# Kernel optimization log

Measured on AMD Instinct MI355X. Metric: run time of the kernel, lower is better.

## Reference

```python
import jax, jax.numpy as jnp
import numpy as np

HEAD_NUM = 16
SCALE = 1.0 / np.sqrt(HEAD_NUM)  # source divides by sqrt(head_num), not head_dim
MASK_VAL = -10000000.0


def setup_inputs() -> dict:
    key = jax.random.key(0)
    kq, kk, kv = jax.random.split(key, 3)
    shape = (2, 16, 2048, 64)  # [B, H, L, D]
    Q = jax.random.normal(kq, shape, dtype=jnp.float32)
    K = jax.random.normal(kk, shape, dtype=jnp.float32)
    V = jax.random.normal(kv, shape, dtype=jnp.float32)
    return {"Q": Q, "K": K, "V": V}


def reference(Q, K, V):
    L = Q.shape[-2]
    # [B, H, L, M] attention logits, scaled by 1/sqrt(head_num)
    logits = jnp.einsum('bhld,bhmd->bhlm', Q, K) * SCALE
    # causal mask: strictly-upper triangle gets -1e7 (additive, as in source)
    mask = jnp.triu(jnp.ones((L, L), dtype=logits.dtype), 1) * MASK_VAL
    logits = logits + mask[None, None, :, :]
    weights = jax.nn.softmax(logits, axis=-1)
    return jnp.einsum('bhlm,bhmd->bhld', weights, V)
```

## Files before the change

kernel.cpp:

```cpp
#include <hip/hip_runtime.h>
#include <hip/hip_bf16.h>

#define BM 128
#define BN 64
#define HD 64
#define LQ 2048
#define SD 72

typedef __attribute__((ext_vector_type(8))) short short8;
typedef __attribute__((ext_vector_type(16))) float f32x16;

#define QSCALE 0.360673760222241f

#define WS_HALF  ((size_t)32 * 2048 * 64)
#define WS_NEEDED (2 * WS_HALF * sizeof(unsigned short))

static __device__ __forceinline__ unsigned pk2(float a, float b) {
    union { __hip_bfloat162 h2; unsigned u; } c;
    c.h2 = __float22bfloat162_rn(make_float2(a, b));
    return c.u;
}

__global__ __launch_bounds__(256)
void prep(const float* __restrict__ Kg, const float* __restrict__ Vg,
          unsigned short* __restrict__ KF, unsigned short* __restrict__ VF) {
    __shared__ unsigned short sK2[64][72];
    __shared__ unsigned short sV2[64][72];
    const int t  = threadIdx.x;
    const int bx = blockIdx.x;
    const int bh = bx >> 5;
    const int c  = bx & 31;
    const size_t ibase = (size_t)bh * (LQ * HD) + (size_t)c * 64 * HD;
    const int r  = t >> 4;
    const int c4 = (t & 15) * 4;

#pragma unroll
    for (int p = 0; p < 4; ++p) {
        const int row = p * 16 + r;
        const float4 kv4 = *(const float4*)(Kg + ibase + (size_t)row * HD + c4);
        uint2 ku; ku.x = pk2(kv4.x, kv4.y); ku.y = pk2(kv4.z, kv4.w);
        *(uint2*)&sK2[row][c4] = ku;
        const float4 vv4 = *(const float4*)(Vg + ibase + (size_t)row * HD + c4);
        const unsigned u0 = pk2(vv4.x, vv4.y);
        const unsigned u1 = pk2(vv4.z, vv4.w);
        sV2[c4 + 0][row] = (unsigned short)(u0 & 0xffff);
        sV2[c4 + 1][row] = (unsigned short)(u0 >> 16);
        sV2[c4 + 2][row] = (unsigned short)(u1 & 0xffff);
        sV2[c4 + 3][row] = (unsigned short)(u1 >> 16);
    }
    __syncthreads();

    const int lane = t & 63;
    const int u    = t >> 6;
    const int l31  = lane & 31;
    const int hh   = lane >> 5;
#pragma unroll
    for (int e = 0; e < 2; ++e) {
        const int ch = 2 * c + e;
        const size_t ob = ((size_t)(bh * 64 + ch) * 4 + u) * 512 + lane * 8;
        *(uint4*)&KF[ob] = *(const uint4*)&sK2[e * 32 + l31][u * 16 + hh * 8];
        *(uint4*)&VF[ob] = *(const uint4*)&sV2[(u & 1) * 32 + l31][e * 32 + (u >> 1) * 16 + hh * 8];
    }
}

__global__ __launch_bounds__(512, 4)
void fa_main(const float* __restrict__ Qg,
             const unsigned short* __restrict__ KF,
             const unsigned short* __restrict__ VF,
             float* __restrict__ Og) {
    __shared__ float fx[4 * 64 * 32];
    __shared__ float fla[4 * 32];

    const int t    = threadIdx.x;
    const int w    = t >> 6;
    const int lane = t & 63;
    const int h    = lane >> 5;
    const int l31  = lane & 31;
    const int qg   = w & 3;
    const int kp   = w >> 2;

    const int bx  = blockIdx.x;
    const int bh  = (bx & 7) * 4 + ((bx >> 3) & 3);
    const int g   = bx >> 5;
    const int qt  = (g < 8) ? (15 - g) : (g - 8);

    const size_t base = (size_t)bh * (LQ * HD);
    const unsigned short* KFh = KF + (size_t)bh * 131072 + lane * 8;
    const unsigned short* VFh = VF + (size_t)bh * 131072 + lane * 8;

    const int j    = 4 * qt + qg;
    const int qrow = j * 32 + l31;

    short8 qreg[4];
    {
        const float* Qrow = Qg + base + (size_t)qrow * HD;
#pragma unroll
        for (int ks = 0; ks < 4; ++ks) {
            const float4 a = *(const float4*)(Qrow + ks * 16 + h * 8);
            const float4 b = *(const float4*)(Qrow + ks * 16 + h * 8 + 4);
            union { unsigned u[4]; short8 s8; } qu;
            qu.u[0] = pk2(a.x * QSCALE, a.y * QSCALE);
            qu.u[1] = pk2(a.z * QSCALE, a.w * QSCALE);
            qu.u[2] = pk2(b.x * QSCALE, b.y * QSCALE);
            qu.u[3] = pk2(b.z * QSCALE, b.w * QSCALE);
            qreg[ks] = qu.s8;
        }
    }

    f32x16 accO[2];
#pragma unroll
    for (int r = 0; r < 16; ++r) { accO[0][r] = 0.f; accO[1][r] = 0.f; }
    float lsum = 0.f;

    short8 ak[4], av[4], pf[2];
    f32x16 accS;

    auto loadK = [&](int ch) {
        const unsigned short* p = KFh + (size_t)ch * 2048;
        ak[0] = *(const short8*)(p);
        ak[1] = *(const short8*)(p + 512);
        ak[2] = *(const short8*)(p + 1024);
        ak[3] = *(const short8*)(p + 1536);
    };
    auto loadV = [&](int ch) {
        const unsigned short* p = VFh + (size_t)ch * 2048;
        av[0] = *(const short8*)(p);
        av[1] = *(const short8*)(p + 512);
        av[2] = *(const short8*)(p + 1024);
        av[3] = *(const short8*)(p + 1536);
    };
    auto qkt = [&]() {
#pragma unroll
        for (int r = 0; r < 16; ++r) accS[r] = 0.f;
        __builtin_amdgcn_s_setprio(1);
#pragma unroll
        for (int ks = 0; ks < 4; ++ks)
            accS = __builtin_amdgcn_mfma_f32_32x32x16_bf16(ak[ks], qreg[ks], accS, 0, 0, 0);
        __builtin_amdgcn_s_setprio(0);
    };
    auto smpk = [&](int pc) {
        if (pc == j) {
            const int kvb = pc * 32 + 4 * h;
#pragma unroll
            for (int r = 0; r < 16; ++r) {
                const int kv = kvb + (r & 3) + 8 * (r >> 2);
                if (kv > qrow) accS[r] = -1e30f;
            }
        }
#pragma unroll
        for (int r = 0; r < 16; ++r) {
            const float p = __builtin_amdgcn_exp2f(accS[r]);
            accS[r] = p;
            lsum += p;
        }
#pragma unroll
        for (int s = 0; s < 2; ++s) {
            const int rb = s * 8;
            const unsigned a0 = pk2(accS[rb + 0], accS[rb + 1]);
            const unsigned b0 = pk2(accS[rb + 4], accS[rb + 5]);
            const unsigned a1 = pk2(accS[rb + 2], accS[rb + 3]);
            const unsigned b1 = pk2(accS[rb + 6], accS[rb + 7]);
            const auto r02 = __builtin_amdgcn_permlane32_swap(a0, b0, 0, 0);
            const auto r13 = __builtin_amdgcn_permlane32_swap(a1, b1, 0, 0);
            union { unsigned u[4]; short8 s8; } pu;
            pu.u[0] = r02[0]; pu.u[1] = r13[0]; pu.u[2] = r02[1]; pu.u[3] = r13[1];
            pf[s] = pu.s8;
        }
    };
    auto pv = [&]() {
        __builtin_amdgcn_s_setprio(1);
#pragma unroll
        for (int s = 0; s < 2; ++s)
#pragma unroll
            for (int dg = 0; dg < 2; ++dg)
                accO[dg] = __builtin_amdgcn_mfma_f32_32x32x16_bf16(av[s * 2 + dg], pf[s], accO[dg], 0, 0, 0);
        __builtin_amdgcn_s_setprio(0);
    };

    int ch = kp;
    if (ch <= j) {
        loadK(ch);
        loadV(ch);
        qkt();
        int pc = ch;
        ch += 2;
        while (ch <= j) {
            loadK(ch);
            __builtin_amdgcn_sched_barrier(0);
            smpk(pc);
            pv();
            loadV(ch);
            __builtin_amdgcn_sched_barrier(0);
            qkt();
            pc = ch;
            ch += 2;
        }
        smpk(pc);
        pv();
    }

    lsum += __shfl_xor(lsum, 32);
    if (kp == 1) {
#pragma unroll
        for (int dg = 0; dg < 2; ++dg) {
#pragma unroll
            for (int r = 0; r < 16; ++r) {
                const int d = dg * 32 + (r & 3) + 8 * (r >> 2) + 4 * h;
                fx[(qg * 64 + d) * 32 + l31] = accO[dg][r];
            }
        }
        if (h == 0) fla[qg * 32 + l31] = lsum;
    }
    __syncthreads();
    if (kp == 0) {
        const float inv = 1.0f / (lsum + fla[qg * 32 + l31]);
        float* Op = Og + base + (size_t)qrow * HD;
#pragma unroll
        for (int dg = 0; dg < 2; ++dg) {
#pragma unroll
            for (int rq = 0; rq < 4; ++rq) {
                const int d = dg * 32 + 8 * rq + 4 * h;
                const float* fr = &fx[(qg * 64 + d) * 32 + l31];
                float4 o;
                o.x = (accO[dg][rq * 4 + 0] + fr[0])  * inv;
                o.y = (accO[dg][rq * 4 + 1] + fr[32]) * inv;
                o.z = (accO[dg][rq * 4 + 2] + fr[64]) * inv;
                o.w = (accO[dg][rq * 4 + 3] + fr[96]) * inv;
                *(float4*)(Op + d) = o;
            }
        }
    }
}

__global__ __launch_bounds__(512, 4)
void fa_fwd(const float* __restrict__ Qg,
            const float* __restrict__ Kg,
            const float* __restrict__ Vg,
            float* __restrict__ Og) {
    __shared__ __align__(16) unsigned short lds[(2 * BN + 2 * HD) * SD];
    typedef unsigned short KT[BN][SD];
    typedef unsigned short VT[HD][SD];
    KT* sK  = (KT*)lds;
    VT* sVt = (VT*)(lds + 2 * BN * SD);

    const int t    = threadIdx.x;
    const int w    = t >> 6;
    const int lane = t & 63;
    const int h    = lane >> 5;
    const int l31  = lane & 31;
    const int qd   = lane >> 4;
    const int qg   = w & 3;
    const int kh   = w >> 2;

    const int bx  = blockIdx.x;
    const int idx = (bx >> 5) & 7;
    const int qt  = (bx & 256) ? idx : (15 - idx);
    const int bh  = bx & 31;
    const int q0  = qt * BM;

    const size_t base = (size_t)bh * (LQ * HD);
    const float* Qp = Qg + base + (size_t)q0 * HD;
    const float* Kp = Kg + base;
    const float* Vp = Vg + base;

    const int r0 = t >> 4;
    const int c4 = (t & 15) * 4;
    const int RA = w * 4;

    {
        unsigned short (*sQ)[SD] = (unsigned short (*)[SD])lds;
#pragma unroll
        for (int p = 0; p < 4; ++p) {
            const int r = p * 32 + r0;
            const float4 v = *(const float4*)(Qp + (size_t)r * HD + c4);
            uint2 u;
            u.x = pk2(v.x * QSCALE, v.y * QSCALE);
            u.y = pk2(v.z * QSCALE, v.w * QSCALE);
            *(uint2*)&sQ[r][c4] = u;
        }
    }
    __syncthreads();
    short8 qreg[4];
    {
        unsigned short (*sQ)[SD] = (unsigned short (*)[SD])lds;
#pragma unroll
        for (int ks = 0; ks < 4; ++ks)
            qreg[ks] = *(const short8*)&sQ[qg * 32 + l31][ks * 16 + h * 8];
    }
    __syncthreads();

    float4 kA, kB, vA, vB;
    auto issue = [&](int kv0) {
        kA = *(const float4*)(Kp + (size_t)(kv0 + r0) * HD + c4);
        kB = *(const float4*)(Kp + (size_t)(kv0 + 32 + r0) * HD + c4);
        vA = *(const float4*)(Vp + (size_t)(kv0 + RA + qd) * HD + c4);
        vB = *(const float4*)(Vp + (size_t)(kv0 + 32 + RA + qd) * HD + c4);
    };
    auto vstore = [&](float4 vf, int R, int buf) {
        float e0 = vf.x, e1 = vf.y, e2 = vf.z, e3 = vf.w;
        float s0 = (qd & 2) ? e0 : e2;
        float s1 = (qd & 2) ? e1 : e3;
        s0 = __shfl_xor(s0, 32); s1 = __shfl_xor(s1, 32);
        if (qd & 2) { e0 = s0; e1 = s1; } else { e2 = s0; e3 = s1; }
        s0 = (qd & 1) ? e0 : e1;
        s1 = (qd & 1) ? e2 : e3;
        s0 = __shfl_xor(s0, 16); s1 = __shfl_xor(s1, 16);
        if (qd & 1) { e0 = s0; e2 = s1; } else { e1 = s0; e3 = s1; }
        const int d   = c4 + qd;
        const int col = ((((R >> 3) ^ (d >> 3)) & 7) << 3) | (R & 7);
        uint2 u; u.x = pk2(e0, e1); u.y = pk2(e2, e3);
        *(uint2*)&sVt[buf][d][col] = u;
    };
    auto commit = [&](int buf) {
        { uint2 u; u.x = pk2(kA.x, kA.y); u.y = pk2(kA.z, kA.w);
          *(uint2*)&sK[buf][r0][c4] = u; }
        { uint2 u; u.x = pk2(kB.x, kB.y); u.y = pk2(kB.z, kB.w);
          *(uint2*)&sK[buf][32 + r0][c4] = u; }
        vstore(vA, RA, buf);
        vstore(vB, 32 + RA, buf);
    };

    f32x16 accO[2];
#pragma unroll
    for (int r = 0; r < 16; ++r) { accO[0][r] = 0.f; accO[1][r] = 0.f; }
    float lsum = 0.f;

    const int qminw = q0 + qg * 32;
    const int qmaxw = qminw + 31;
    const int n_it  = (q0 + BM) / BN;

    issue(0);
    commit(0);

    for (int it = 0; it < n_it; ++it) {
        const int kv0 = it * BN;
        const int buf = it & 1;
        __syncthreads();
        const bool more = (it + 1 < n_it);
        if (more) issue(kv0 + BN);

        if (kv0 + kh * 32 <= qmaxw) {
            f32x16 accS;
#pragma unroll
            for (int r = 0; r < 16; ++r) accS[r] = 0.f;
            __builtin_amdgcn_s_setprio(1);
#pragma unroll
            for (int ks = 0; ks < 4; ++ks) {
                const short8 ak = *(const short8*)&sK[buf][kh * 32 + l31][ks * 16 + h * 8];
                accS = __builtin_amdgcn_mfma_f32_32x32x16_bf16(ak, qreg[ks], accS, 0, 0, 0);
            }
            __builtin_amdgcn_s_setprio(0);

            if (kv0 + kh * 32 + 31 > qminw) {
                const int qrow = qminw + l31;
                const int kvb  = kv0 + kh * 32 + 4 * h;
#pragma unroll
                for (int r = 0; r < 16; ++r) {
                    const int kv = kvb + (r & 3) + 8 * (r >> 2);
                    if (kv > qrow) accS[r] = -1e30f;
                }
            }
#pragma unroll
            for (int r = 0; r < 16; ++r) {
                const float p = __builtin_amdgcn_exp2f(accS[r]);
                accS[r] = p;
                lsum += p;
            }
            short8 pf[2];
#pragma unroll
            for (int s = 0; s < 2; ++s) {
                const int rb = s * 8;
                const unsigned a0 = pk2(accS[rb + 0], accS[rb + 1]);
                const unsigned b0 = pk2(accS[rb + 4], accS[rb + 5]);
                const unsigned a1 = pk2(accS[rb + 2], accS[rb + 3]);
                const unsigned b1 = pk2(accS[rb + 6], accS[rb + 7]);
                const auto r02 = __builtin_amdgcn_permlane32_swap(a0, b0, 0, 0);
                const auto r13 = __builtin_amdgcn_permlane32_swap(a1, b1, 0, 0);
                union { unsigned u[4]; short8 s8; } pu;
                pu.u[0] = r02[0]; pu.u[1] = r13[0]; pu.u[2] = r02[1]; pu.u[3] = r13[1];
                pf[s] = pu.s8;
            }
            __builtin_amdgcn_s_setprio(1);
#pragma unroll
            for (int s = 0; s < 2; ++s) {
                const int K0 = kh * 32 + s * 16 + h * 8;
#pragma unroll
                for (int dg = 0; dg < 2; ++dg) {
                    const int d   = dg * 32 + l31;
                    const int col = (((K0 >> 3) ^ (d >> 3)) & 7) << 3;
                    const short8 av = *(const short8*)&sVt[buf][d][col];
                    accO[dg] = __builtin_amdgcn_mfma_f32_32x32x16_bf16(av, pf[s], accO[dg], 0, 0, 0);
                }
            }
            __builtin_amdgcn_s_setprio(0);
        }

        if (more) commit(buf ^ 1);
    }

    lsum += __shfl_xor(lsum, 32);
    __syncthreads();
    float* fx  = (float*)lds;
    float* fla = fx + 4 * 64 * 32;
    if (kh == 1) {
#pragma unroll
        for (int dg = 0; dg < 2; ++dg) {
#pragma unroll
            for (int r = 0; r < 16; ++r) {
                const int d = dg * 32 + (r & 3) + 8 * (r >> 2) + 4 * h;
                fx[(qg * 64 + d) * 32 + l31] = accO[dg][r];
            }
        }
        if (h == 0) fla[qg * 32 + l31] = lsum;
    }
    __syncthreads();
    if (kh == 0) {
        const float inv  = 1.0f / (lsum + fla[qg * 32 + l31]);
        const int   qrow = q0 + qg * 32 + l31;
        float* Op = Og + base + (size_t)qrow * HD;
#pragma unroll
        for (int dg = 0; dg < 2; ++dg) {
#pragma unroll
            for (int rq = 0; rq < 4; ++rq) {
                const int d = dg * 32 + 8 * rq + 4 * h;
                const float* fr = &fx[(qg * 64 + d) * 32 + l31];
                float4 o;
                o.x = (accO[dg][rq * 4 + 0] + fr[0])  * inv;
                o.y = (accO[dg][rq * 4 + 1] + fr[32]) * inv;
                o.z = (accO[dg][rq * 4 + 2] + fr[64]) * inv;
                o.w = (accO[dg][rq * 4 + 3] + fr[96]) * inv;
                *(float4*)(Op + d) = o;
            }
        }
    }
}

extern "C" void kernel_launch(void* const* d_in, const int* in_sizes, int n_in,
                              void* d_out, int out_size, void* d_ws, size_t ws_size,
                              hipStream_t stream) {
    const float* Q = (const float*)d_in[0];
    const float* K = (const float*)d_in[1];
    const float* V = (const float*)d_in[2];
    float* O = (float*)d_out;
    if (d_ws != nullptr && ws_size >= WS_NEEDED) {
        unsigned short* KF = (unsigned short*)d_ws;
        unsigned short* VF = KF + WS_HALF;
        prep<<<dim3(1024), dim3(256), 0, stream>>>(K, V, KF, VF);
        fa_main<<<dim3(512), dim3(512), 0, stream>>>(Q, KF, VF, O);
    } else {
        fa_fwd<<<dim3(512), dim3(512), 0, stream>>>(Q, K, V, O);
    }
}
```

Baseline: 118.7 us.

## Rebalance causal work: pair mirrored query tiles per block, split KV four ways

Each block now handles two query groups per segment, with four warps per group splitting the KV chunks at stride 4 instead of two. It processes two mirrored 32-row query tiles, j and 63-j, in sequence, so every block does roughly equal causal work. Partial outputs from three KV-split warps are reduced through a larger shared buffer. The lsum accumulation is split into two chains to shorten the dependency. This removes the load imbalance of causal tiles and the old tile-ordering heuristic, but adds an extra LDS reduction, a second barrier per segment and a larger shared-memory footprint, which may lower occupancy.

```diff
diff --git a/kernel.cpp b/kernel.cpp
--- a/kernel.cpp
+++ b/kernel.cpp
@@ -68,52 +68,30 @@
              const unsigned short* __restrict__ KF,
              const unsigned short* __restrict__ VF,
              float* __restrict__ Og) {
-    __shared__ float fx[4 * 64 * 32];
-    __shared__ float fla[4 * 32];
+    __shared__ float fx[2 * 3 * 64 * 32];
+    __shared__ float fla[2 * 3 * 32];
 
     const int t    = threadIdx.x;
     const int w    = t >> 6;
     const int lane = t & 63;
     const int h    = lane >> 5;
     const int l31  = lane & 31;
-    const int qg   = w & 3;
-    const int kp   = w >> 2;
+    const int qg   = w & 1;
+    const int kp   = w >> 1;
 
     const int bx  = blockIdx.x;
-    const int bh  = (bx & 7) * 4 + ((bx >> 3) & 3);
+    const int bh  = bx & 31;
     const int g   = bx >> 5;
-    const int qt  = (g < 8) ? (15 - g) : (g - 8);
+    const int js  = 2 * g + qg;
 
     const size_t base = (size_t)bh * (LQ * HD);
     const unsigned short* KFh = KF + (size_t)bh * 131072 + lane * 8;
     const unsigned short* VFh = VF + (size_t)bh * 131072 + lane * 8;
 
-    const int j    = 4 * qt + qg;
-    const int qrow = j * 32 + l31;
-
-    short8 qreg[4];
-    {
-        const float* Qrow = Qg + base + (size_t)qrow * HD;
-#pragma unroll
-        for (int ks = 0; ks < 4; ++ks) {
-            const float4 a = *(const float4*)(Qrow + ks * 16 + h * 8);
-            const float4 b = *(const float4*)(Qrow + ks * 16 + h * 8 + 4);
-            union { unsigned u[4]; short8 s8; } qu;
-            qu.u[0] = pk2(a.x * QSCALE, a.y * QSCALE);
-            qu.u[1] = pk2(a.z * QSCALE, a.w * QSCALE);
-            qu.u[2] = pk2(b.x * QSCALE, b.y * QSCALE);
-            qu.u[3] = pk2(b.z * QSCALE, b.w * QSCALE);
-            qreg[ks] = qu.s8;
-        }
-    }
-
-    f32x16 accO[2];
-#pragma unroll
-    for (int r = 0; r < 16; ++r) { accO[0][r] = 0.f; accO[1][r] = 0.f; }
-    float lsum = 0.f;
-
-    short8 ak[4], av[4], pf[2];
-    f32x16 accS;
+    short8 qreg[4], ak[4], av[4], pf[2];
+    f32x16 accS, accO[2];
+    float lsum0, lsum1;
+    int j, qrow;
 
     auto loadK = [&](int ch) {
         const unsigned short* p = KFh + (size_t)ch * 2048;
@@ -151,7 +129,7 @@
         for (int r = 0; r < 16; ++r) {
             const float p = __builtin_amdgcn_exp2f(accS[r]);
             accS[r] = p;
-            lsum += p;
+            if (r & 1) lsum1 += p; else lsum0 += p;
         }
 #pragma unroll
         for (int s = 0; s < 2; ++s) {
@@ -177,58 +155,90 @@
         __builtin_amdgcn_s_setprio(0);
     };
 
-    int ch = kp;
-    if (ch <= j) {
-        loadK(ch);
-        loadV(ch);
-        qkt();
-        int pc = ch;
-        ch += 2;
-        while (ch <= j) {
+#pragma unroll 1
+    for (int seg = 0; seg < 2; ++seg) {
+        j    = seg ? (63 - js) : js;
+        qrow = j * 32 + l31;
+
+        {
+            const float* Qrow = Qg + base + (size_t)qrow * HD;
+#pragma unroll
+            for (int ks = 0; ks < 4; ++ks) {
+                const float4 a = *(const float4*)(Qrow + ks * 16 + h * 8);
+                const float4 b = *(const float4*)(Qrow + ks * 16 + h * 8 + 4);
+                union { unsigned u[4]; short8 s8; } qu;
+                qu.u[0] = pk2(a.x * QSCALE, a.y * QSCALE);
+                qu.u[1] = pk2(a.z * QSCALE, a.w * QSCALE);
+                qu.u[2] = pk2(b.x * QSCALE, b.y * QSCALE);
+                qu.u[3] = pk2(b.z * QSCALE, b.w * QSCALE);
+                qreg[ks] = qu.s8;
+            }
+        }
+#pragma unroll
+        for (int r = 0; r < 16; ++r) { accO[0][r] = 0.f; accO[1][r] = 0.f; }
+        lsum0 = 0.f; lsum1 = 0.f;
+
+        int ch = kp;
+        if (ch <= j) {
             loadK(ch);
-            __builtin_amdgcn_sched_barrier(0);
+            loadV(ch);
+            qkt();
+            int pc = ch;
+            ch += 4;
+            while (ch <= j) {
+                loadK(ch);
+                __builtin_amdgcn_sched_barrier(0);
+                smpk(pc);
+                pv();
+                loadV(ch);
+                __builtin_amdgcn_sched_barrier(0);
+                qkt();
+                pc = ch;
+                ch += 4;
+            }
             smpk(pc);
             pv();
-            loadV(ch);
-            __builtin_amdgcn_sched_barrier(0);
-            qkt();
-            pc = ch;
-            ch += 2;
-        }
-        smpk(pc);
-        pv();
-    }
-
-    lsum += __shfl_xor(lsum, 32);
-    if (kp == 1) {
-#pragma unroll
-        for (int dg = 0; dg < 2; ++dg) {
-#pragma unroll
-            for (int r = 0; r < 16; ++r) {
-                const int d = dg * 32 + (r & 3) + 8 * (r >> 2) + 4 * h;
-                fx[(qg * 64 + d) * 32 + l31] = accO[dg][r];
-            }
-        }
-        if (h == 0) fla[qg * 32 + l31] = lsum;
-    }
-    __syncthreads();
-    if (kp == 0) {
-        const float inv = 1.0f / (lsum + fla[qg * 32 + l31]);
-        float* Op = Og + base + (size_t)qrow * HD;
-#pragma unroll
-        for (int dg = 0; dg < 2; ++dg) {
-#pragma unroll
-            for (int rq = 0; rq < 4; ++rq) {
-                const int d = dg * 32 + 8 * rq + 4 * h;
-                const float* fr = &fx[(qg * 64 + d) * 32 + l31];
-                float4 o;
-                o.x = (accO[dg][rq * 4 + 0] + fr[0])  * inv;
-                o.y = (accO[dg][rq * 4 + 1] + fr[32]) * inv;
-                o.z = (accO[dg][rq * 4 + 2] + fr[64]) * inv;
-                o.w = (accO[dg][rq * 4 + 3] + fr[96]) * inv;
-                *(float4*)(Op + d) = o;
-            }
-        }
+        }
+
+        float lsum = lsum0 + lsum1;
+        lsum += __shfl_xor(lsum, 32);
+        if (kp != 0) {
+            const int kpi = kp - 1;
+#pragma unroll
+            for (int dg = 0; dg < 2; ++dg) {
+#pragma unroll
+                for (int r = 0; r < 16; ++r) {
+                    const int d = dg * 32 + (r & 3) + 8 * (r >> 2) + 4 * h;
+                    fx[(((qg * 3 + kpi) * 64) + d) * 32 + l31] = accO[dg][r];
+                }
+            }
+            if (h == 0) fla[(qg * 3 + kpi) * 32 + l31] = lsum;
+        }
+        __syncthreads();
+        if (kp == 0) {
+            const float den = lsum + fla[(qg * 3 + 0) * 32 + l31]
+                                   + fla[(qg * 3 + 1) * 32 + l31]
+                                   + fla[(qg * 3 + 2) * 32 + l31];
+            const float inv = 1.0f / den;
+            float* Op = Og + base + (size_t)qrow * HD;
+#pragma unroll
+            for (int dg = 0; dg < 2; ++dg) {
+#pragma unroll
+                for (int rq = 0; rq < 4; ++rq) {
+                    const int d = dg * 32 + 8 * rq + 4 * h;
+                    const float* f0 = &fx[(((qg * 3 + 0) * 64) + d) * 32 + l31];
+                    const float* f1 = &fx[(((qg * 3 + 1) * 64) + d) * 32 + l31];
+                    const float* f2 = &fx[(((qg * 3 + 2) * 64) + d) * 32 + l31];
+                    float4 o;
+                    o.x = (accO[dg][rq * 4 + 0] + f0[0]  + f1[0]  + f2[0])  * inv;
+                    o.y = (accO[dg][rq * 4 + 1] + f0[32] + f1[32] + f2[32]) * inv;
+                    o.z = (accO[dg][rq * 4 + 2] + f0[64] + f1[64] + f2[64]) * inv;
+                    o.w = (accO[dg][rq * 4 + 3] + f0[96] + f1[96] + f2[96]) * inv;
+                    *(float4*)(Op + d) = o;
+                }
+            }
+        }
+        __syncthreads();
     }
 }
 
```

After: 137.3 us. 1.16x slower.
